# Performance work log

Measured on AMD Instinct MI355X. Metric: run time of the kernel, lower is better.

Reference implementation:

```python
import jax, jax.numpy as jnp
import numpy as np

EPS = 1e-8
BETA = 1.0
NUM_ITEM = 100000
DIM = 256
NUM_SETS = 8192
SET_LEN = 50
BATCH = 131072


def _init_table(key, clamp_min=None):
    w = 0.1 * jax.random.normal(key, (NUM_ITEM, DIM), dtype=jnp.float32)
    nrm = jnp.linalg.norm(w, axis=1, keepdims=True)
    w = w / jnp.maximum(nrm, 1.0)
    if clamp_min is not None:
        w = jnp.maximum(w, clamp_min)
    return w


def setup_inputs() -> dict:
    key = jax.random.key(0)
    ks = jax.random.split(key, 8)
    S = jax.random.randint(ks[0], (NUM_SETS, SET_LEN), 0, NUM_ITEM, dtype=jnp.int64 if jax.config.jax_enable_x64 else jnp.int32)
    M = jax.random.randint(ks[1], (NUM_SETS, SET_LEN), 0, 2, dtype=jnp.int32)
    instances = jax.random.randint(ks[2], (BATCH, 2), 0, NUM_SETS, dtype=jnp.int32)
    similarities = jax.random.uniform(ks[3], (BATCH, 4), dtype=jnp.float32)
    stdv = 1.0 / np.sqrt(DIM)
    center_att = jax.random.uniform(ks[4], (DIM,), minval=-stdv, maxval=stdv, dtype=jnp.float32)
    radius_att = jax.random.uniform(ks[5], (DIM,), minval=-stdv, maxval=stdv, dtype=jnp.float32)
    center_w = _init_table(ks[6])
    radius_w = _init_table(ks[7], clamp_min=EPS)
    return {"S": S, "M": M, "instances": instances, "similarities": similarities,
            "center_w": center_w, "radius_w": radius_w,
            "center_att": center_att, "radius_att": radius_att}


def _softplus_beta(x):
    # f.softplus(x, beta) = log(1 + exp(beta*x)) / beta
    return jax.nn.softplus(BETA * x) / BETA


def _attention_ber(S, M, X, A):
    # Dense masked equivalent of nonzero() + scatter_softmax + scatter_sum.
    att = X @ A                              # [num_item]
    logits = att[S]                          # [num_sets, L]
    mask = M > 0
    logits = jnp.where(mask, logits, -1e30)
    w = jax.nn.softmax(logits, axis=1)       # [num_sets, L]
    w = jnp.where(mask, w, 0.0)
    emb = jnp.einsum('sl,sld->sd', w, X[S])  # [num_sets, D]
    sizes = jnp.sum(M, axis=1).astype(X.dtype)  # set sizes
    emb = emb * (sizes[:, None] ** (1.0 / DIM))  # size_reg=True for both
    return emb


def reference(S, M, instances, similarities, center_w, radius_w, center_att, radius_att):
    emb_c_all = _attention_ber(S, M, center_w, center_att)   # [num_sets, D]
    emb_r_all = _attention_ber(S, M, radius_w, radius_att)   # [num_sets, D]
    emb_center = emb_c_all[instances]  # [B, 2, D]
    emb_radius = emb_r_all[instances]  # [B, 2, D]

    c_i, c_j = emb_center[:, 0, :], emb_center[:, 1, :]
    r_i, r_j = emb_radius[:, 0, :], emb_radius[:, 1, :]
    m_i, m_j = c_i, c_j
    M_i, M_j = c_i + r_i, c_j + r_j

    box_volume_i = jnp.sum(jnp.log(_softplus_beta(r_i) + EPS), axis=1)
    box_volume_j = jnp.sum(jnp.log(_softplus_beta(r_j) + EPS), axis=1)
    box_volume_mul_ij = box_volume_i + box_volume_j
    box_inter = jnp.sum(jnp.log(_softplus_beta(jnp.minimum(M_i, M_j) - jnp.maximum(m_i, m_j)) + EPS), axis=1)
    box_union = jnp.sum(jnp.log(_softplus_beta(jnp.maximum(M_i, M_j) - jnp.minimum(m_i, m_j)) + EPS), axis=1)

    c_overlap = jnp.exp(box_inter - jnp.maximum(box_volume_i, box_volume_j))
    c_jaccard = jnp.exp(box_inter - box_union)
    c_cosine = jnp.exp(box_inter - box_volume_mul_ij / 2)
    c_dice = 2 * jnp.exp(box_inter) / (jnp.exp(box_volume_i) + jnp.exp(box_volume_j) + EPS)

    lose_1 = jnp.sum((c_overlap - similarities[:, 0]) ** 2)
    lose_2 = jnp.sum((c_jaccard - similarities[:, 1]) ** 2)
    lose_3 = jnp.sum((c_cosine - similarities[:, 2]) ** 2)
    lose_4 = jnp.sum((c_dice - similarities[:, 3]) ** 2)
    return (lose_1, lose_2, lose_3, lose_4)
```

## Files before the change

kernel.cpp:

```cpp
#include <hip/hip_runtime.h>

#define EPSF 1e-8f
#define DIM 256
#define SET_LEN 50
#define NUM_SETS 8192
#define BATCH 131072

#define LOG2E 1.4426950408889634f
#define LN2   0.6931471805599453f
#define EPS2  1.4426950409e-8f
#define CPD  -0.5287663729448977f

#define QSCALE 100.0f
#define QINV   0.01f
#define Q2E    (QINV * LOG2E)
#define LUTOFF 204
#define LUTSZ  512

#define PPW 16
#define NPAIRBLK (BATCH / (PPW * 4))

__device__ __forceinline__ float fast_exp2(float x) {
#if __has_builtin(__builtin_amdgcn_exp2f)
    return __builtin_amdgcn_exp2f(x);
#else
    return exp2f(x);
#endif
}
__device__ __forceinline__ float fast_log2(float x) {
#if __has_builtin(__builtin_amdgcn_logf)
    return __builtin_amdgcn_logf(x);
#else
    return __log2f(x);
#endif
}

__device__ __forceinline__ float lsp2(float x) {
    float e = fast_exp2(x * LOG2E);
    float s = fast_log2(1.0f + e);
    return fast_log2(s + EPS2);
}
__device__ __forceinline__ float lsp2q(int q) {
    float e = fast_exp2((float)q * Q2E);
    float s = fast_log2(1.0f + e);
    return fast_log2(s + EPS2);
}

__device__ __forceinline__ float wave_reduce_sum(float v) {
    #pragma unroll
    for (int off = 32; off > 0; off >>= 1) v += __shfl_xor(v, off, 64);
    return v;
}
__device__ __forceinline__ float wave_reduce_max(float v) {
    #pragma unroll
    for (int off = 32; off > 0; off >>= 1) v = fmaxf(v, __shfl_xor(v, off, 64));
    return v;
}

__device__ __forceinline__ unsigned short f32_to_bf16(float f) {
    unsigned int u = __float_as_uint(f);
    unsigned int r = (u + 0x7fffu + ((u >> 16) & 1u)) >> 16;
    return (unsigned short)r;
}
__device__ __forceinline__ uint2 pack_bf16x4(float4 v) {
    uint2 r;
    r.x = (unsigned int)f32_to_bf16(v.x) | ((unsigned int)f32_to_bf16(v.y) << 16);
    r.y = (unsigned int)f32_to_bf16(v.z) | ((unsigned int)f32_to_bf16(v.w) << 16);
    return r;
}
__device__ __forceinline__ float bf16_ld(const unsigned short* p) {
    return __uint_as_float((unsigned int)(*p) << 16);
}

__device__ __forceinline__ float dot4(float4 a, float4 b) {
    return a.x*b.x + a.y*b.y + a.z*b.z + a.w*b.w;
}

__device__ __forceinline__ signed char quant8(float v) {
    int q = (int)rintf(v * QSCALE);
    q = max(-127, min(127, q));
    return (signed char)q;
}

__global__ __launch_bounds__(256) void attn_kernel(
    const int* __restrict__ S, const int* __restrict__ M,
    const float* __restrict__ Xc, const float* __restrict__ Xr,
    const float* __restrict__ Ac, const float* __restrict__ Ar,
    signed char* __restrict__ emb_q, float* __restrict__ bv)
{
    const int s    = blockIdx.x;
    const int tid  = threadIdx.x;
    const int lane = tid & 63;
    const int wid  = tid >> 6;
    const int g    = lane >> 4;
    const int sl   = lane & 15;

    __shared__ unsigned short shc[SET_LEN][DIM];
    __shared__ unsigned short shr[SET_LEN][DIM];
    __shared__ int   sh_act[SET_LEN];
    __shared__ float sh_logc[SET_LEN];
    __shared__ float sh_logr[SET_LEN];
    __shared__ float sh_wc[SET_LEN];
    __shared__ float sh_wr[SET_LEN];
    __shared__ int   sh_nact;
    __shared__ float sh_scale;
    __shared__ float sh_red[4];

    if (wid == 0) {
        int idx = 0, m = 0;
        if (lane < SET_LEN) {
            idx = S[s * SET_LEN + lane];
            m   = M[s * SET_LEN + lane];
        }
        unsigned long long bal = __ballot(m != 0);
        int rank = __popcll(bal & ((1ull << lane) - 1ull));
        if (m) sh_act[rank] = idx;
        if (lane == 0) {
            int n = __popcll(bal);
            sh_nact = n;
            sh_scale = (n > 0) ? exp2f(log2f((float)n) * (1.0f / DIM)) : 0.0f;
        }
    }
    __syncthreads();
    const int nact = sh_nact;

    float4 afc[4], afr[4];
    #pragma unroll
    for (int c = 0; c < 4; ++c) {
        afc[c] = ((const float4*)Ac)[c * 16 + sl];
        afr[c] = ((const float4*)Ar)[c * 16 + sl];
    }

    const int nit = (nact + 15) >> 4;
    for (int it = 0; it < nit; ++it) {
        const int k = it * 16 + wid * 4 + g;
        float pc = 0.0f, pr = 0.0f;
        if (k < nact) {
            const size_t row = (size_t)sh_act[k] * DIM;
            const float4* xc = (const float4*)(Xc + row);
            const float4* xr = (const float4*)(Xr + row);
            float4 c0 = xc[sl], c1 = xc[16 + sl], c2 = xc[32 + sl], c3 = xc[48 + sl];
            float4 r0 = xr[sl], r1 = xr[16 + sl], r2 = xr[32 + sl], r3 = xr[48 + sl];
            pc = dot4(c0, afc[0]) + dot4(c1, afc[1]) + dot4(c2, afc[2]) + dot4(c3, afc[3]);
            pr = dot4(r0, afr[0]) + dot4(r1, afr[1]) + dot4(r2, afr[2]) + dot4(r3, afr[3]);
            *(uint2*)&shc[k][  0 + 4*sl] = pack_bf16x4(c0);
            *(uint2*)&shc[k][ 64 + 4*sl] = pack_bf16x4(c1);
            *(uint2*)&shc[k][128 + 4*sl] = pack_bf16x4(c2);
            *(uint2*)&shc[k][192 + 4*sl] = pack_bf16x4(c3);
            *(uint2*)&shr[k][  0 + 4*sl] = pack_bf16x4(r0);
            *(uint2*)&shr[k][ 64 + 4*sl] = pack_bf16x4(r1);
            *(uint2*)&shr[k][128 + 4*sl] = pack_bf16x4(r2);
            *(uint2*)&shr[k][192 + 4*sl] = pack_bf16x4(r3);
        }
        #pragma unroll
        for (int off = 8; off > 0; off >>= 1) {
            pc += __shfl_xor(pc, off, 64);
            pr += __shfl_xor(pr, off, 64);
        }
        if (k < nact && sl == 0) { sh_logc[k] = pc; sh_logr[k] = pr; }
    }
    __syncthreads();

    if (wid < 2) {
        float* lg = (wid == 0) ? sh_logc : sh_logr;
        float* w  = (wid == 0) ? sh_wc  : sh_wr;
        float v  = (lane < nact) ? lg[lane] : -1e30f;
        float mx = wave_reduce_max(v);
        float p  = (lane < nact) ? __expf(v - mx) : 0.0f;
        float sm = wave_reduce_sum(p);
        float inv = (sm > 0.0f) ? (1.0f / sm) : 0.0f;
        if (lane < nact) w[lane] = p * inv;
    }
    __syncthreads();

    float accc = 0.0f, accr = 0.0f;
    #pragma unroll 4
    for (int k = 0; k < nact; ++k) {
        accc = fmaf(sh_wc[k], bf16_ld(&shc[k][tid]), accc);
        accr = fmaf(sh_wr[k], bf16_ld(&shr[k][tid]), accr);
    }
    const float scale = sh_scale;
    const float ec = accc * scale;
    const float er = accr * scale;
    emb_q[(size_t)s * 512 + tid]       = quant8(ec);
    emb_q[(size_t)s * 512 + 256 + tid] = quant8(er);

    float term = lsp2(er);
    float wsum = wave_reduce_sum(term);
    if (lane == 0) sh_red[wid] = wsum;
    __syncthreads();
    if (tid == 0)
        bv[s] = LN2 * ((sh_red[0] + sh_red[1] + sh_red[2] + sh_red[3])
                       + (float)DIM * CPD);
}

__device__ __forceinline__ void i8x16_unpack(uint4 u, int* o) {
    unsigned int ws[4] = { u.x, u.y, u.z, u.w };
    #pragma unroll
    for (int w = 0; w < 4; ++w) {
        o[4*w+0] = (int)(signed char)(ws[w]);
        o[4*w+1] = (int)(signed char)(ws[w] >> 8);
        o[4*w+2] = (int)(signed char)(ws[w] >> 16);
        o[4*w+3] = (int)(signed char)(ws[w] >> 24);
    }
}

__device__ __forceinline__ void pair_accum_lut(const float* __restrict__ lut,
                                               uint4 ac, uint4 ar, uint4 bc, uint4 br,
                                               float& it, float& ut) {
    int ci[16], ri[16], cj[16], rj[16];
    i8x16_unpack(ac, ci); i8x16_unpack(ar, ri);
    i8x16_unpack(bc, cj); i8x16_unpack(br, rj);
    #pragma unroll
    for (int k = 0; k < 16; ++k) {
        const int Mi = ci[k] + ri[k];
        const int Mj = cj[k] + rj[k];
        const int lo = min(Mi, Mj) - max(ci[k], cj[k]);
        const int hi = max(Mi, Mj) - min(ci[k], cj[k]);
        it += lut[lo + LUTOFF];
        ut += lut[hi + LUTOFF];
    }
}

__global__ __launch_bounds__(256) void pair_kernel(
    const int* __restrict__ inst, const float* __restrict__ sims,
    const signed char* __restrict__ emb_q,
    const float* __restrict__ bv, float4* __restrict__ part)
{
    const int tid  = threadIdx.x;
    const int lane = tid & 63;
    const int wid  = tid >> 6;
    const int g    = lane >> 4;
    const int sl   = lane & 15;
    const int wave = blockIdx.x * 4 + wid;
    const int base = wave * PPW;

    __shared__ float lut[LUTSZ];
    __shared__ float sh_i[4][PPW];
    __shared__ float sh_u[4][PPW];
    __shared__ float sred[4][4];

    #pragma unroll
    for (int e = tid; e < LUTSZ; e += 256) lut[e] = lsp2q(e - LUTOFF);

    int idxreg = 0;
    if (lane < 2 * PPW) idxreg = inst[2 * base + lane];
    __syncthreads();

    uint4 a_c, a_r, b_c, b_r;
    {
        const int i = __shfl(idxreg, 2 * g);
        const int j = __shfl(idxreg, 2 * g + 1);
        const uint4* pi = (const uint4*)(emb_q + (size_t)i * 512);
        const uint4* pj = (const uint4*)(emb_q + (size_t)j * 512);
        a_c = pi[sl]; a_r = pi[16 + sl];
        b_c = pj[sl]; b_r = pj[16 + sl];
    }

    #pragma unroll
    for (int m = 0; m < 4; ++m) {
        uint4 n0, n1, n2, n3;
        if (m < 3) {
            const int slot = (m + 1) * 4 + g;
            const int i = __shfl(idxreg, 2 * slot);
            const int j = __shfl(idxreg, 2 * slot + 1);
            const uint4* pi = (const uint4*)(emb_q + (size_t)i * 512);
            const uint4* pj = (const uint4*)(emb_q + (size_t)j * 512);
            n0 = pi[sl]; n1 = pi[16 + sl];
            n2 = pj[sl]; n3 = pj[16 + sl];
        }

        float it = 0.0f, ut = 0.0f;
        pair_accum_lut(lut, a_c, a_r, b_c, b_r, it, ut);
        #pragma unroll
        for (int o = 8; o > 0; o >>= 1) {
            it += __shfl_xor(it, o, 64);
            ut += __shfl_xor(ut, o, 64);
        }
        if (sl == 0) { sh_i[wid][m * 4 + g] = it; sh_u[wid][m * 4 + g] = ut; }

        if (m < 3) { a_c = n0; a_r = n1; b_c = n2; b_r = n3; }
    }
    __syncthreads();

    float l1 = 0.0f, l2 = 0.0f, l3 = 0.0f, l4 = 0.0f;
    if (lane < PPW) {
        const int b = base + lane;
        const int i = inst[2 * b];
        const int j = inst[2 * b + 1];
        const float inter = LN2 * (sh_i[wid][lane] + (float)DIM * CPD);
        const float unn   = LN2 * (sh_u[wid][lane] + (float)DIM * CPD);
        const float bvi = bv[i], bvj = bv[j];
        const float co  = __expf(inter - fmaxf(bvi, bvj));
        const float cja = __expf(inter - unn);
        const float cco = __expf(inter - 0.5f * (bvi + bvj));
        const float cdi = 2.0f * __expf(inter) /
                          (__expf(bvi) + __expf(bvj) + EPSF);
        const float4 sm = ((const float4*)sims)[b];
        float d;
        d = co  - sm.x; l1 = d * d;
        d = cja - sm.y; l2 = d * d;
        d = cco - sm.z; l3 = d * d;
        d = cdi - sm.w; l4 = d * d;
    }
    l1 = wave_reduce_sum(l1);
    l2 = wave_reduce_sum(l2);
    l3 = wave_reduce_sum(l3);
    l4 = wave_reduce_sum(l4);

    if (lane == 0) {
        sred[wid][0] = l1; sred[wid][1] = l2;
        sred[wid][2] = l3; sred[wid][3] = l4;
    }
    __syncthreads();
    if (tid == 0) {
        float4 p;
        p.x = sred[0][0] + sred[1][0] + sred[2][0] + sred[3][0];
        p.y = sred[0][1] + sred[1][1] + sred[2][1] + sred[3][1];
        p.z = sred[0][2] + sred[1][2] + sred[2][2] + sred[3][2];
        p.w = sred[0][3] + sred[1][3] + sred[2][3] + sred[3][3];
        part[blockIdx.x] = p;
    }
}

__global__ __launch_bounds__(256) void reduce_out(
    const float4* __restrict__ part, float* __restrict__ out)
{
    const int tid  = threadIdx.x;
    const int lane = tid & 63;
    const int wid  = tid >> 6;

    double s0 = 0.0, s1 = 0.0, s2 = 0.0, s3 = 0.0;
    for (int k = tid; k < NPAIRBLK; k += 256) {
        float4 p = part[k];
        s0 += (double)p.x; s1 += (double)p.y;
        s2 += (double)p.z; s3 += (double)p.w;
    }
    #pragma unroll
    for (int off = 32; off > 0; off >>= 1) {
        s0 += __shfl_xor(s0, off, 64);
        s1 += __shfl_xor(s1, off, 64);
        s2 += __shfl_xor(s2, off, 64);
        s3 += __shfl_xor(s3, off, 64);
    }
    __shared__ double sd[4][4];
    if (lane == 0) { sd[wid][0] = s0; sd[wid][1] = s1; sd[wid][2] = s2; sd[wid][3] = s3; }
    __syncthreads();
    if (tid == 0) {
        out[0] = (float)(sd[0][0] + sd[1][0] + sd[2][0] + sd[3][0]);
        out[1] = (float)(sd[0][1] + sd[1][1] + sd[2][1] + sd[3][1]);
        out[2] = (float)(sd[0][2] + sd[1][2] + sd[2][2] + sd[3][2]);
        out[3] = (float)(sd[0][3] + sd[1][3] + sd[2][3] + sd[3][3]);
    }
}

extern "C" void kernel_launch(void* const* d_in, const int* in_sizes, int n_in,
                              void* d_out, int out_size, void* d_ws, size_t ws_size,
                              hipStream_t stream) {
    const int*   S    = (const int*)d_in[0];
    const int*   M    = (const int*)d_in[1];
    const int*   inst = (const int*)d_in[2];
    const float* sims = (const float*)d_in[3];
    const float* Xc   = (const float*)d_in[4];
    const float* Xr   = (const float*)d_in[5];
    const float* Ac   = (const float*)d_in[6];
    const float* Ar   = (const float*)d_in[7];
    float* out = (float*)d_out;

    char* ws = (char*)d_ws;
    signed char* emb_q = (signed char*)(ws);
    float*  bv   = (float*)(ws + 4194304);
    float4* part = (float4*)(ws + 4227072);

    attn_kernel<<<NUM_SETS, 256, 0, stream>>>(S, M, Xc, Xr, Ac, Ar, emb_q, bv);
    pair_kernel<<<NPAIRBLK, 256, 0, stream>>>(inst, sims, emb_q, bv, part);
    reduce_out<<<1, 256, 0, stream>>>(part, out);
}
```

Measured before the change: 90.70 us.

## Fuse set attention softmax into streaming online-softmax accumulation in registers

Replaces the staging of gathered rows into shared memory as bf16, the separate softmax pass and the weighted-sum pass with a single streaming online-softmax loop. Each 16-lane group keeps a running max, sum and fp32 embedding accumulator. Groups are merged via shuffles and a small shared-memory combine across waves. This cuts shared memory use sharply, which should raise occupancy for the memory-bound gather, and removes two barriers, at the cost of more registers and extra exp work per row.

```diff
diff --git a/kernel.cpp b/kernel.cpp
--- a/kernel.cpp
+++ b/kernel.cpp
@@ -51,35 +51,35 @@
     for (int off = 32; off > 0; off >>= 1) v += __shfl_xor(v, off, 64);
     return v;
 }
-__device__ __forceinline__ float wave_reduce_max(float v) {
-    #pragma unroll
-    for (int off = 32; off > 0; off >>= 1) v = fmaxf(v, __shfl_xor(v, off, 64));
-    return v;
-}
 
 __device__ __forceinline__ unsigned short f32_to_bf16(float f) {
     unsigned int u = __float_as_uint(f);
     unsigned int r = (u + 0x7fffu + ((u >> 16) & 1u)) >> 16;
     return (unsigned short)r;
 }
-__device__ __forceinline__ uint2 pack_bf16x4(float4 v) {
-    uint2 r;
-    r.x = (unsigned int)f32_to_bf16(v.x) | ((unsigned int)f32_to_bf16(v.y) << 16);
-    r.y = (unsigned int)f32_to_bf16(v.z) | ((unsigned int)f32_to_bf16(v.w) << 16);
-    return r;
-}
-__device__ __forceinline__ float bf16_ld(const unsigned short* p) {
-    return __uint_as_float((unsigned int)(*p) << 16);
-}
-
 __device__ __forceinline__ float dot4(float4 a, float4 b) {
     return a.x*b.x + a.y*b.y + a.z*b.z + a.w*b.w;
 }
-
 __device__ __forceinline__ signed char quant8(float v) {
     int q = (int)rintf(v * QSCALE);
     q = max(-127, min(127, q));
     return (signed char)q;
+}
+__device__ __forceinline__ float4 f4_axpby(float4 e, float a, float4 x, float w) {
+    float4 r;
+    r.x = fmaf(e.x, a, x.x * w);
+    r.y = fmaf(e.y, a, x.y * w);
+    r.z = fmaf(e.z, a, x.z * w);
+    r.w = fmaf(e.w, a, x.w * w);
+    return r;
+}
+__device__ __forceinline__ float4 shfl_xor_f4(float4 v, int off) {
+    float4 r;
+    r.x = __shfl_xor(v.x, off, 64);
+    r.y = __shfl_xor(v.y, off, 64);
+    r.z = __shfl_xor(v.z, off, 64);
+    r.w = __shfl_xor(v.w, off, 64);
+    return r;
 }
 
 __global__ __launch_bounds__(256) void attn_kernel(
@@ -95,15 +95,12 @@
     const int g    = lane >> 4;
     const int sl   = lane & 15;
 
-    __shared__ unsigned short shc[SET_LEN][DIM];
-    __shared__ unsigned short shr[SET_LEN][DIM];
     __shared__ int   sh_act[SET_LEN];
-    __shared__ float sh_logc[SET_LEN];
-    __shared__ float sh_logr[SET_LEN];
-    __shared__ float sh_wc[SET_LEN];
-    __shared__ float sh_wr[SET_LEN];
     __shared__ int   sh_nact;
     __shared__ float sh_scale;
+    __shared__ float Ec_l[4][DIM];
+    __shared__ float Er_l[4][DIM];
+    __shared__ float m4c[4], s4c[4], m4r[4], s4r[4];
     __shared__ float sh_red[4];
 
     if (wid == 0) {
@@ -131,57 +128,118 @@
         afr[c] = ((const float4*)Ar)[c * 16 + sl];
     }
 
-    const int nit = (nact + 15) >> 4;
-    for (int it = 0; it < nit; ++it) {
-        const int k = it * 16 + wid * 4 + g;
-        float pc = 0.0f, pr = 0.0f;
-        if (k < nact) {
-            const size_t row = (size_t)sh_act[k] * DIM;
-            const float4* xc = (const float4*)(Xc + row);
-            const float4* xr = (const float4*)(Xr + row);
-            float4 c0 = xc[sl], c1 = xc[16 + sl], c2 = xc[32 + sl], c3 = xc[48 + sl];
-            float4 r0 = xr[sl], r1 = xr[16 + sl], r2 = xr[32 + sl], r3 = xr[48 + sl];
-            pc = dot4(c0, afc[0]) + dot4(c1, afc[1]) + dot4(c2, afc[2]) + dot4(c3, afc[3]);
-            pr = dot4(r0, afr[0]) + dot4(r1, afr[1]) + dot4(r2, afr[2]) + dot4(r3, afr[3]);
-            *(uint2*)&shc[k][  0 + 4*sl] = pack_bf16x4(c0);
-            *(uint2*)&shc[k][ 64 + 4*sl] = pack_bf16x4(c1);
-            *(uint2*)&shc[k][128 + 4*sl] = pack_bf16x4(c2);
-            *(uint2*)&shc[k][192 + 4*sl] = pack_bf16x4(c3);
-            *(uint2*)&shr[k][  0 + 4*sl] = pack_bf16x4(r0);
-            *(uint2*)&shr[k][ 64 + 4*sl] = pack_bf16x4(r1);
-            *(uint2*)&shr[k][128 + 4*sl] = pack_bf16x4(r2);
-            *(uint2*)&shr[k][192 + 4*sl] = pack_bf16x4(r3);
-        }
+    float mc = -1e30f, sc = 0.0f, mr = -1e30f, sr = 0.0f;
+    float4 Ec[4], Er[4];
+    #pragma unroll
+    for (int c = 0; c < 4; ++c) {
+        Ec[c] = make_float4(0.f, 0.f, 0.f, 0.f);
+        Er[c] = make_float4(0.f, 0.f, 0.f, 0.f);
+    }
+
+    for (int k = wid * 4 + g; k < nact; k += 16) {
+        const size_t row = (size_t)sh_act[k] * DIM;
+        const float4* xc = (const float4*)(Xc + row);
+        const float4* xr = (const float4*)(Xr + row);
+        float4 c0 = xc[sl], c1 = xc[16 + sl], c2 = xc[32 + sl], c3 = xc[48 + sl];
+        float4 r0 = xr[sl], r1 = xr[16 + sl], r2 = xr[32 + sl], r3 = xr[48 + sl];
+
+        float pc = dot4(c0, afc[0]) + dot4(c1, afc[1]) + dot4(c2, afc[2]) + dot4(c3, afc[3]);
+        float pr = dot4(r0, afr[0]) + dot4(r1, afr[1]) + dot4(r2, afr[2]) + dot4(r3, afr[3]);
         #pragma unroll
         for (int off = 8; off > 0; off >>= 1) {
             pc += __shfl_xor(pc, off, 64);
             pr += __shfl_xor(pr, off, 64);
         }
-        if (k < nact && sl == 0) { sh_logc[k] = pc; sh_logr[k] = pr; }
-    }
-    __syncthreads();
-
-    if (wid < 2) {
-        float* lg = (wid == 0) ? sh_logc : sh_logr;
-        float* w  = (wid == 0) ? sh_wc  : sh_wr;
-        float v  = (lane < nact) ? lg[lane] : -1e30f;
-        float mx = wave_reduce_max(v);
-        float p  = (lane < nact) ? __expf(v - mx) : 0.0f;
-        float sm = wave_reduce_sum(p);
-        float inv = (sm > 0.0f) ? (1.0f / sm) : 0.0f;
-        if (lane < nact) w[lane] = p * inv;
-    }
-    __syncthreads();
-
-    float accc = 0.0f, accr = 0.0f;
-    #pragma unroll 4
-    for (int k = 0; k < nact; ++k) {
-        accc = fmaf(sh_wc[k], bf16_ld(&shc[k][tid]), accc);
-        accr = fmaf(sh_wr[k], bf16_ld(&shr[k][tid]), accr);
-    }
+
+        {
+            float mn = fmaxf(mc, pc);
+            float rs = fast_exp2((mc - mn) * LOG2E);
+            float w  = fast_exp2((pc - mn) * LOG2E);
+            sc = fmaf(sc, rs, w);
+            Ec[0] = f4_axpby(Ec[0], rs, c0, w);
+            Ec[1] = f4_axpby(Ec[1], rs, c1, w);
+            Ec[2] = f4_axpby(Ec[2], rs, c2, w);
+            Ec[3] = f4_axpby(Ec[3], rs, c3, w);
+            mc = mn;
+        }
+        {
+            float mn = fmaxf(mr, pr);
+            float rs = fast_exp2((mr - mn) * LOG2E);
+            float w  = fast_exp2((pr - mn) * LOG2E);
+            sr = fmaf(sr, rs, w);
+            Er[0] = f4_axpby(Er[0], rs, r0, w);
+            Er[1] = f4_axpby(Er[1], rs, r1, w);
+            Er[2] = f4_axpby(Er[2], rs, r2, w);
+            Er[3] = f4_axpby(Er[3], rs, r3, w);
+            mr = mn;
+        }
+    }
+
+    #pragma unroll
+    for (int off = 16; off <= 32; off <<= 1) {
+        {
+            float mo = __shfl_xor(mc, off, 64);
+            float so = __shfl_xor(sc, off, 64);
+            float mn = fmaxf(mc, mo);
+            float ra = fast_exp2((mc - mn) * LOG2E);
+            float rb = fast_exp2((mo - mn) * LOG2E);
+            #pragma unroll
+            for (int c = 0; c < 4; ++c) {
+                float4 Eo = shfl_xor_f4(Ec[c], off);
+                Ec[c] = f4_axpby(Ec[c], ra, Eo, rb);
+            }
+            sc = fmaf(sc, ra, so * rb);
+            mc = mn;
+        }
+        {
+            float mo = __shfl_xor(mr, off, 64);
+            float so = __shfl_xor(sr, off, 64);
+            float mn = fmaxf(mr, mo);
+            float ra = fast_exp2((mr - mn) * LOG2E);
+            float rb = fast_exp2((mo - mn) * LOG2E);
+            #pragma unroll
+            for (int c = 0; c < 4; ++c) {
+                float4 Eo = shfl_xor_f4(Er[c], off);
+                Er[c] = f4_axpby(Er[c], ra, Eo, rb);
+            }
+            sr = fmaf(sr, ra, so * rb);
+            mr = mn;
+        }
+    }
+
+    if (lane < 16) {
+        #pragma unroll
+        for (int c = 0; c < 4; ++c) {
+            ((float4*)&Ec_l[wid][0])[c * 16 + sl] = Ec[c];
+            ((float4*)&Er_l[wid][0])[c * 16 + sl] = Er[c];
+        }
+    }
+    if (lane == 0) { m4c[wid] = mc; s4c[wid] = sc; m4r[wid] = mr; s4r[wid] = sr; }
+    __syncthreads();
+
     const float scale = sh_scale;
-    const float ec = accc * scale;
-    const float er = accr * scale;
+    float ec, er;
+    {
+        float m1 = fmaxf(fmaxf(m4c[0], m4c[1]), fmaxf(m4c[2], m4c[3]));
+        float w0 = fast_exp2((m4c[0] - m1) * LOG2E);
+        float w1 = fast_exp2((m4c[1] - m1) * LOG2E);
+        float w2 = fast_exp2((m4c[2] - m1) * LOG2E);
+        float w3 = fast_exp2((m4c[3] - m1) * LOG2E);
+        float den = s4c[0]*w0 + s4c[1]*w1 + s4c[2]*w2 + s4c[3]*w3;
+        float num = Ec_l[0][tid]*w0 + Ec_l[1][tid]*w1 + Ec_l[2][tid]*w2 + Ec_l[3][tid]*w3;
+        ec = (den > 0.0f) ? (num / den) * scale : 0.0f;
+    }
+    {
+        float m1 = fmaxf(fmaxf(m4r[0], m4r[1]), fmaxf(m4r[2], m4r[3]));
+        float w0 = fast_exp2((m4r[0] - m1) * LOG2E);
+        float w1 = fast_exp2((m4r[1] - m1) * LOG2E);
+        float w2 = fast_exp2((m4r[2] - m1) * LOG2E);
+        float w3 = fast_exp2((m4r[3] - m1) * LOG2E);
+        float den = s4r[0]*w0 + s4r[1]*w1 + s4r[2]*w2 + s4r[3]*w3;
+        float num = Er_l[0][tid]*w0 + Er_l[1][tid]*w1 + Er_l[2][tid]*w2 + Er_l[3][tid]*w3;
+        er = (den > 0.0f) ? (num / den) * scale : 0.0f;
+    }
+
     emb_q[(size_t)s * 512 + tid]       = quant8(ec);
     emb_q[(size_t)s * 512 + 256 + tid] = quant8(er);
 
```

Measured after the change: 98.15 us. 1.08x slower.
